# Performance work log

Measured on AMD Instinct MI355X. Metric: run time of the kernel, lower is better.

## Reference

```python
import jax, jax.numpy as jnp
import numpy as np

N_HEADS = 8
EPS = 1e-8


def _build_gp_map():
    # Cl(4,1) geometric-product structure constants. Blade index = 5-bit mask,
    # e1..e5 = bits 0..4; metric (+,+,+,+,-): e5 (bit 4) squares to -1.
    def pc(n):
        return bin(n).count("1")
    g = np.zeros((32, 32, 32), np.float32)
    for a in range(32):
        for b in range(32):
            swaps = 0
            aa = a >> 1
            while aa:
                swaps += pc(aa & b)
                aa >>= 1
            sign = -1.0 if (swaps & 1) else 1.0
            if (a & b) & 0b10000:  # shared e5 factor contributes -1
                sign = -sign
            g[a, b, a ^ b] = sign
    return g

GP_MAP = jnp.asarray(_build_gp_map())          # (32,32,32)
BIVEC_IDX = jnp.array([3, 5, 6, 9, 10, 12, 17, 18, 20, 24])  # grade-2 blades
SCALAR_VECTOR_IDX = np.array([0, 1, 2, 4, 8, 16])            # grade-0 + grade-1


def normalize_cl41(x):
    return x / jnp.sqrt(jnp.sum(x * x, axis=-1, keepdims=True) + EPS)


def geometric_linear(w, x):
    # w: (O,I,32), x: (...,I,32) -> (...,O,32)
    wg = jnp.einsum('oij,jlk->oilk', w, GP_MAP)     # fold gp_map into weight
    out = jnp.einsum('oilk,...il->...ok', wg, x)
    return normalize_cl41(out)


def _init_weight(key, out_f, in_f):
    # Grade-aware Xavier: only scalar + vector lanes are nonzero.
    std = 1.0 / np.sqrt(in_f * 32)
    vals = jax.random.normal(key, (out_f, in_f, len(SCALAR_VECTOR_IDX)), jnp.float32) * std
    w = jnp.zeros((out_f, in_f, 32), jnp.float32)
    return w.at[:, :, SCALAR_VECTOR_IDX].set(vals)


def setup_inputs() -> dict:
    key = jax.random.key(0)
    kx, kq, kk, kv, ko = jax.random.split(key, 5)
    B, S, D = 2, 384, 128
    x = jax.random.normal(kx, (B, S, D, 32), jnp.float32)
    return {
        'x': x,
        'wq': _init_weight(kq, D, D),
        'wk': _init_weight(kk, D, D),
        'wv': _init_weight(kv, D, D),
        'wo': _init_weight(ko, D, D),
        'attn_lambda': jnp.float32(0.1),
    }


def reference(x, wq, wk, wv, wo, attn_lambda):
    B, S, D, _ = x.shape
    H = N_HEADS
    hd = D // H
    def split_heads(t):  # (B,S,D,32) -> (B,H,S,hd,32)
        return t.reshape(B, S, H, hd, 32).transpose(0, 2, 1, 3, 4)
    q = split_heads(geometric_linear(wq, x))
    k = split_heads(geometric_linear(wk, x))
    v = split_heads(geometric_linear(wv, x))

    # Geometric product Q*K contracted over head_dim, then over gp_map lanes.
    qg = jnp.einsum('bhsdi,ijk->bhsdjk', q, GP_MAP)      # (B,H,S,hd,32,32)
    raw_mv = jnp.einsum('bhsdjk,bhxdj->bhsxk', qg, k)    # (B,H,S,S,32)
    raw_mv = normalize_cl41(raw_mv)

    scalar_part = raw_mv[..., 0]
    biv = raw_mv[..., BIVEC_IDX]
    bivector_norm = jnp.sqrt(jnp.sum(biv * biv, axis=-1) + EPS)
    score = (scalar_part + attn_lambda * bivector_norm) / np.sqrt(hd).astype(np.float32)
    attn_probs = jax.nn.softmax(score, axis=-1)          # (B,H,S,S)

    out = jnp.einsum('bhsx,bhxdl->bhsdl', attn_probs, v)  # (B,H,S,hd,32)
    out = out.transpose(0, 2, 1, 3, 4).reshape(B, S, D, 32)
    return geometric_linear(wo, out)
```

## Files before the change

### kernel.cpp

```cpp
#include <hip/hip_runtime.h>
#include <math.h>

#define BB    2
#define SS    384
#define DD    128
#define NH    8
#define HDIM  16
#define NBH   16
#define BS    768

typedef unsigned int   u32;
typedef unsigned short u16;
typedef __attribute__((ext_vector_type(8))) short short8;
typedef __attribute__((ext_vector_type(4))) float f32x4;

struct SignTab { float v[32][32]; };
constexpr int popcnt32c(int x){ int c=0; for(int i=0;i<32;i++) c += (x>>i)&1; return c; }
constexpr int signgp_int(int a, int b){
  int swaps=0; int aa=a>>1;
  while(aa){ swaps += popcnt32c(aa & b); aa >>= 1; }
  int s = (swaps & 1) ? -1 : 1;
  if ((a & b) & 16) s = -s;
  return s;
}
constexpr SignTab make_signs(){
  SignTab t{};
  for(int a=0;a<32;a++) for(int b=0;b<32;b++)
    t.v[a][b] = (float)signgp_int(a,b);
  return t;
}
constexpr SignTab GPS = make_signs();

struct MaskTab { u32 v[4][8][4][4]; };
constexpr MaskTab mkmask(){
  MaskTab t{};
  for(int w=0;w<4;w++) for(int u=0;u<8;u++) for(int q=0;q<4;q++) for(int r=0;r<4;r++){
    u32 m = 0;
    for(int h=0;h<2;h++){
      int j = 2*r + h;
      int i = (q<<3) | j;
      int c = (w<<3) | u;
      if (signgp_int(i, i^c) < 0) m |= (h ? 0x80000000u : 0x8000u);
    }
    t.v[w][u][q][r] = m;
  }
  return t;
}
constexpr MaskTab MT = mkmask();

__device__ __forceinline__ u16 f2bf(float f){
  u32 x = __float_as_uint(f);
  return (u16)((x + 0x7FFFu + ((x>>16)&1u)) >> 16);
}
__device__ __forceinline__ float bf2f(u16 h){
  return __uint_as_float(((u32)h) << 16);
}

__global__ __launch_bounds__(256) void repack_wb(const float* __restrict__ wq,
                                                 const float* __restrict__ wk,
                                                 const float* __restrict__ wv,
                                                 const float* __restrict__ wo,
                                                 u16* __restrict__ wpk2){
  int idx = blockIdx.x*256 + threadIdx.x;
  int p = blockIdx.y;
  const float* w = (p==0)?wq:(p==1)?wk:(p==2)?wv:wo;
  int o   = idx / 768;
  int rem = idx - o*768;
  int jp  = rem >> 7;
  int i   = rem & 127;
  const int SV[6] = {0,1,2,4,8,16};
  wpk2[p*98304 + idx] = f2bf(w[(o*128 + i)*32 + SV[jp]]);
}

#define XLS 33
__global__ __launch_bounds__(256) void gather_k(const void* __restrict__ src,
                                                int src_bf16,
                                                u16* __restrict__ xg){
  __shared__ float xl[2*128*XLS];
  int t = threadIdx.x;
  int bs0 = blockIdx.x*2;
  int bsl = t >> 7, i = t & 127;

  float row[32];
  if (src_bf16){
    const uint4* s4 = (const uint4*)((const u16*)src + (((size_t)(bs0+bsl)*128 + i)*32));
    #pragma unroll
    for(int r=0;r<4;r++){
      uint4 v = s4[r];
      u32 ww[4] = {v.x,v.y,v.z,v.w};
      #pragma unroll
      for(int h=0;h<4;h++){
        row[r*8 + 2*h    ] = __uint_as_float(ww[h] << 16);
        row[r*8 + 2*h + 1] = __uint_as_float(ww[h] & 0xFFFF0000u);
      }
    }
  } else {
    const float4* s4 = (const float4*)((const float*)src + (((size_t)(bs0+bsl)*128 + i)*32));
    #pragma unroll
    for(int r=0;r<8;r++){
      float4 v = s4[r];
      row[r*4+0]=v.x; row[r*4+1]=v.y; row[r*4+2]=v.z; row[r*4+3]=v.w;
    }
  }
  float* xrow = xl + bsl*128*XLS + i*XLS;
  #pragma unroll
  for(int l=0;l<32;l++) xrow[l] = row[l];
  __syncthreads();

  const int SV[6] = {0,1,2,4,8,16};
  u32* xg32 = (u32*)xg;
  #pragma unroll 4
  for(int r=0;r<96;r++){
    int wr = t + r*256;
    int k   = wr / 768;
    int rem = wr - k*768;
    int bl  = rem / 384;
    int r2  = rem - bl*384;
    int jp  = r2 >> 6;
    int ip  = r2 & 63;
    int i2  = ip*2;
    int b   = SV[jp] ^ k;
    float sg = GPS.v[SV[jp]][b];
    const float* base = xl + bl*128*XLS;
    float f0 = base[ i2   *XLS + b] * sg;
    float f1 = base[(i2+1)*XLS + b] * sg;
    u32 pk = (u32)f2bf(f0) | ((u32)f2bf(f1) << 16);
    xg32[((size_t)k*768 + bs0 + bl)*384 + jp*64 + ip] = pk;
  }
}

#define LSTR 40
__global__ __launch_bounds__(256) void gemm_proj(const u16* __restrict__ xg,
                                                 const u16* __restrict__ wpkA,
                                                 u16* __restrict__ tmpA){
  __shared__ __align__(16) u16 As[128*LSTR];
  __shared__ __align__(16) u16 Bs[128*LSTR];
  int t = threadIdx.x;
  int Mt = blockIdx.x, k = blockIdx.y, p = blockIdx.z;
  const u16* wpk = wpkA + (size_t)p*98304;
  u16* tmp = tmpA + (size_t)p*32*768*128;

  int w = t >> 6, lane = t & 63;
  int q = lane >> 4, n16 = lane & 15;
  int wm = w >> 1, wn = w & 1;

  f32x4 acc[4][4];
  #pragma unroll
  for(int a=0;a<4;a++)
    #pragma unroll
    for(int b=0;b<4;b++) acc[a][b] = (f32x4){0.f,0.f,0.f,0.f};

  int r0 = t>>2, c0 = (t&3)*8;
  int r1 = (t+256)>>2, c1 = ((t+256)&3)*8;
  const u16* Aab = xg + ((size_t)k*768 + Mt*128)*768;

  uint4 pa0, pa1, pb0, pb1;
  {
    pa0 = *(const uint4*)(Aab + (size_t)r0*768 + c0);
    pa1 = *(const uint4*)(Aab + (size_t)r1*768 + c1);
    pb0 = *(const uint4*)(wpk + (size_t)r0*768 + c0);
    pb1 = *(const uint4*)(wpk + (size_t)r1*768 + c1);
  }

  for(int kt=0; kt<24; kt++){
    __syncthreads();
    *(uint4*)(As + r0*LSTR + c0) = pa0;
    *(uint4*)(As + r1*LSTR + c1) = pa1;
    *(uint4*)(Bs + r0*LSTR + c0) = pb0;
    *(uint4*)(Bs + r1*LSTR + c1) = pb1;
    __syncthreads();
    if (kt < 23){
      int kn = (kt+1)*32;
      pa0 = *(const uint4*)(Aab + (size_t)r0*768 + kn + c0);
      pa1 = *(const uint4*)(Aab + (size_t)r1*768 + kn + c1);
      pb0 = *(const uint4*)(wpk + (size_t)r0*768 + kn + c0);
      pb1 = *(const uint4*)(wpk + (size_t)r1*768 + kn + c1);
    }
    short8 a[4], b[4];
    #pragma unroll
    for(int mi=0;mi<4;mi++)
      a[mi] = *(const short8*)(As + (wm*64 + mi*16 + n16)*LSTR + q*8);
    #pragma unroll
    for(int ni=0;ni<4;ni++)
      b[ni] = *(const short8*)(Bs + (wn*64 + ni*16 + n16)*LSTR + q*8);
    #pragma unroll
    for(int mi=0;mi<4;mi++)
      #pragma unroll
      for(int ni=0;ni<4;ni++)
        acc[mi][ni] = __builtin_amdgcn_mfma_f32_16x16x32_bf16(a[mi], b[ni], acc[mi][ni], 0,0,0);
  }

  #pragma unroll
  for(int mi=0;mi<4;mi++){
    #pragma unroll
    for(int r=0;r<4;r++){
      int m = Mt*128 + wm*64 + mi*16 + q*4 + r;
      #pragma unroll
      for(int ni=0;ni<4;ni++){
        int n = wn*64 + ni*16 + n16;
        tmp[((size_t)k*768 + m)*128 + n] = f2bf(acc[mi][ni][r]);
      }
    }
  }
}

__global__ __launch_bounds__(256) void norm3(const u16* __restrict__ tmpA,
                                             u16* __restrict__ qhb,
                                             u16* __restrict__ khb,
                                             u16* __restrict__ vbb){
  int z = blockIdx.y;
  const u16* tmp = tmpA + (size_t)z*32*768*128;
  u16* dst = (z==0)?qhb:(z==1)?khb:vbb;
  int t = threadIdx.x;
  int bsl = t >> 7, o = t & 127;
  int bs = blockIdx.x*2 + bsl;

  float a[32];
  float ssum = 1e-8f;
  #pragma unroll
  for(int k=0;k<32;k++){
    a[k] = bf2f(tmp[((size_t)k*768 + bs)*128 + o]);
    ssum = fmaf(a[k], a[k], ssum);
  }
  float inv = 1.0f / sqrtf(ssum);

  int b = bs / SS, s = bs - b*SS;
  int h = o >> 4, d = o & 15;
  uint4* og4 = (uint4*)(dst + (((size_t)(b*NH + h)*SS + s)*512 + d*32));
  #pragma unroll
  for(int l=0;l<4;l++){
    uint4 v;
    v.x = (u32)f2bf(a[8*l+0]*inv) | ((u32)f2bf(a[8*l+1]*inv)<<16);
    v.y = (u32)f2bf(a[8*l+2]*inv) | ((u32)f2bf(a[8*l+3]*inv)<<16);
    v.z = (u32)f2bf(a[8*l+4]*inv) | ((u32)f2bf(a[8*l+5]*inv)<<16);
    v.w = (u32)f2bf(a[8*l+6]*inv) | ((u32)f2bf(a[8*l+7]*inv)<<16);
    og4[l] = v;
  }
}

__global__ __launch_bounds__(256) void norm_out(const u16* __restrict__ tmp,
                                                float* __restrict__ dst){
  int t = threadIdx.x;
  int bsl = t >> 7, o = t & 127;
  int bs = blockIdx.x*2 + bsl;

  float a[32];
  float ssum = 1e-8f;
  #pragma unroll
  for(int k=0;k<32;k++){
    a[k] = bf2f(tmp[((size_t)k*768 + bs)*128 + o]);
    ssum = fmaf(a[k], a[k], ssum);
  }
  float inv = 1.0f / sqrtf(ssum);
  float4* og = (float4*)(dst + ((size_t)bs*128 + o)*32);
  #pragma unroll
  for(int l4=0;l4<8;l4++){
    float4 v;
    v.x = a[4*l4+0]*inv; v.y = a[4*l4+1]*inv;
    v.z = a[4*l4+2]*inv; v.w = a[4*l4+3]*inv;
    og[l4] = v;
  }
}

#define TVS 528
__global__ __launch_bounds__(256) void transpose_v(const u16* __restrict__ vb,
                                                   u16* __restrict__ vt){
  __shared__ __align__(16) u16 vl[32*TVS];
  int t = threadIdx.x;
  int xt = blockIdx.x, bh = blockIdx.y;
  const u16* src = vb + ((size_t)bh*SS + xt*32)*512;
  #pragma unroll
  for(int j=0;j<8;j++){
    int f = t + j*256; int row = f>>6, c = (f&63)*8;
    *(uint4*)(vl + row*TVS + c) = *(const uint4*)(src + (size_t)row*512 + c);
  }
  __syncthreads();
  u16* dst = vt + (size_t)bh*512*SS + xt*32;
  #pragma unroll
  for(int j=0;j<8;j++){
    int f = t + j*256; int dl = f>>2, c4 = (f&3)*8;
    u16 tmp[8];
    #pragma unroll
    for(int e=0;e<8;e++) tmp[e] = vl[(c4+e)*TVS + dl];
    *(uint4*)(dst + (size_t)dl*SS + c4) = *(uint4*)tmp;
  }
}

#define QSTR 264
__global__ __launch_bounds__(256,2) void scores_mfma(const u16* __restrict__ qh,
                                                     const u16* __restrict__ kh,
                                                     float* __restrict__ sc,
                                                     const float* __restrict__ lam){
  __shared__ __align__(16) u16 smem[(64+16)*QSTR];
  u16* qs = smem;
  u16* ks = smem + 64*QSTR;
  int t = threadIdx.x;
  int xt = blockIdx.x, st = blockIdx.y, bh = blockIdx.z;
  int w = t >> 6, lane = t & 63, q = lane >> 4, mn = lane & 15;
  float lm = lam[0];

  u32 FM[8][4];
  #pragma unroll
  for(int u=0;u<8;u++)
    #pragma unroll
    for(int r=0;r<4;r++) FM[u][r] = MT.v[w][u][q][r];

  f32x4 acc[4][8];
  #pragma unroll
  for(int mi=0;mi<4;mi++)
    #pragma unroll
    for(int u=0;u<8;u++) acc[mi][u] = (f32x4){0.f,0.f,0.f,0.f};

  for(int h=0; h<2; h++){
    __syncthreads();
    const u16* qbase = qh + ((size_t)bh*SS + st*64)*512 + h*256;
    const u16* kbase = kh + ((size_t)bh*SS + xt*16)*512 + h*256;
    #pragma unroll
    for(int j=0;j<8;j++){
      int f = t + j*256;
      int row = f>>5, c = (f&31)*8;
      *(uint4*)(qs + row*QSTR + c) = *(const uint4*)(qbase + (size_t)row*512 + c);
    }
    #pragma unroll
    for(int j=0;j<2;j++){
      int f = t + j*256;
      int row = f>>5, c = (f&31)*8;
      *(uint4*)(ks + row*QSTR + c) = *(const uint4*)(kbase + (size_t)row*512 + c);
    }
    __syncthreads();

    for(int ktl=0; ktl<8; ktl++){
      short8 a[4];
      #pragma unroll
      for(int mi=0;mi<4;mi++)
        a[mi] = *(const short8*)(qs + (mi*16+mn)*QSTR + ktl*32 + q*8);
      uint4 khd = *(const uint4*)(ks + mn*QSTR + ktl*32 + ((q^w)<<3));
      u32 kk[4]  = {khd.x, khd.y, khd.z, khd.w};
      u32 kks[4];
      #pragma unroll
      for(int r=0;r<4;r++) kks[r] = (kk[r]>>16)|(kk[r]<<16);
      #pragma unroll
      for(int u=0;u<8;u++){
        union { u32 w32[4]; short8 s; } bf;
        #pragma unroll
        for(int r=0;r<4;r++){
          u32 v = (u & 1) ? kks[r ^ (u>>1)] : kk[r ^ (u>>1)];
          bf.w32[r] = v ^ FM[u][r];
        }
        #pragma unroll
        for(int mi=0;mi<4;mi++)
          acc[mi][u] = __builtin_amdgcn_mfma_f32_16x16x32_bf16(a[mi], bf.s, acc[mi][u], 0, 0, 0);
      }
    }
  }
  __syncthreads();

  float* pss = (float*)smem;
  float* pbb = pss + 64*68;
  float* ps0 = pbb + 64*68;

  #pragma unroll
  for(int mi=0;mi<4;mi++){
    #pragma unroll
    for(int rr=0;rr<4;rr++){
      float ssv = 0.f, bbv = 0.f;
      #pragma unroll
      for(int u=0;u<8;u++){
        int c = w*8 + u;
        bool isb = (c==3)||(c==5)||(c==6)||(c==9)||(c==10)||(c==12)||
                   (c==17)||(c==18)||(c==20)||(c==24);
        float v = acc[mi][u][rr];
        ssv = fmaf(v, v, ssv);
        if (isb) bbv = fmaf(v, v, bbv);
      }
      int s = mi*16 + q*4 + rr;
      pss[s*68 + w*16 + mn] = ssv;
      pbb[s*68 + w*16 + mn] = bbv;
      if (w == 0) ps0[s*17 + mn] = acc[mi][0][rr];
    }
  }
  __syncthreads();

  int x = t & 15, s0 = t >> 4;
  #pragma unroll
  for(int ssi=0; ssi<4; ssi++){
    int s = s0 + ssi*16;
    float ss = 1e-8f, bb = 0.f;
    #pragma unroll
    for(int ww=0; ww<4; ww++){
      ss += pss[s*68 + ww*16 + x];
      bb += pbb[s*68 + ww*16 + x];
    }
    float inv = 1.0f / sqrtf(ss);
    float s0v = ps0[s*17+x];
    float score = (s0v*inv + lm*sqrtf(bb*inv*inv + 1e-8f)) * 0.25f;
    sc[((size_t)bh*SS + st*64 + s)*SS + xt*16 + x] = score;
  }
}

#define PBS 392
#define VSS 40
__global__ __launch_bounds__(256,2) void pv_mfma(const float* __restrict__ sc,
                                                 const u16* __restrict__ vt,
                                                 u16* __restrict__ om){
  __shared__ __align__(16) u16 pb[16*PBS];
  __shared__ __align__(16) u16 vsm[512*VSS];
  int t = threadIdx.x;
  int st = blockIdx.x, bh = blockIdx.y;
  int w = t >> 6, lane = t & 63, q = lane >> 4, mn = lane & 15;

  {
    int row = t >> 4, g = t & 15;
    const float* srow = sc + ((size_t)bh*SS + st*16 + row)*SS;
    float v[24];
    float mx = -1e30f;
    #pragma unroll
    for(int k2=0;k2<24;k2++){ v[k2] = srow[g + k2*16]; mx = fmaxf(mx, v[k2]); }
    #pragma unroll
    for(int off=8; off; off>>=1) mx = fmaxf(mx, __shfl_xor(mx, off));
    float sum = 0.f;
    #pragma unroll
    for(int k2=0;k2<24;k2++){ v[k2] = __expf(v[k2]-mx); sum += v[k2]; }
    #pragma unroll
    for(int off=8; off; off>>=1) sum += __shfl_xor(sum, off);
    float inv = 1.f/sum;
    #pragma unroll
    for(int k2=0;k2<24;k2++) pb[row*PBS + g + k2*16] = f2bf(v[k2]*inv);
  }

  f32x4 acc[8];
  #pragma unroll
  for(int mt=0;mt<8;mt++) acc[mt] = (f32x4){0.f,0.f,0.f,0.f};

  const u16* vtb = vt + (size_t)bh*512*SS;
  for(int kt=0; kt<12; kt++){
    __syncthreads();
    #pragma unroll
    for(int j=0;j<8;j++){
      int f = t + j*256;
      int dl = f>>2, c4 = (f&3)*8;
      *(uint4*)(vsm + dl*VSS + c4) = *(const uint4*)(vtb + (size_t)dl*SS + kt*32 + c4);
    }
    __syncthreads();
    short8 b = *(const short8*)(pb + mn*PBS + kt*32 + q*8);
    #pragma unroll
    for(int mt=0;mt<8;mt++){
      short8 a = *(const short8*)(vsm + ((w*8+mt)*16 + mn)*VSS + q*8);
      acc[mt] = __builtin_amdgcn_mfma_f32_16x16x32_bf16(a, b, acc[mt], 0, 0, 0);
    }
  }
  __syncthreads();

  float* ot = (float*)vsm;
  #pragma unroll
  for(int mt=0;mt<8;mt++)
    #pragma unroll
    for(int rr=0;rr<4;rr++)
      ot[((w*8+mt)*16 + q*4 + rr)*17 + mn] = acc[mt][rr];
  __syncthreads();

  int b = bh >> 3, h = bh & 7;
  u32* om32 = (u32*)om;
  #pragma unroll
  for(int j=0;j<16;j++){
    int f = t + j*256;
    int s = f >> 8, dlp = f & 255, dl = dlp*2;
    float f0 = ot[dl*17 + s], f1 = ot[(dl+1)*17 + s];
    u32 pk = (u32)f2bf(f0) | ((u32)f2bf(f1) << 16);
    int sg = st*16 + s;
    om32[(size_t)(b*SS + sg)*2048 + h*256 + dlp] = pk;
  }
}

extern "C" void kernel_launch(void* const* d_in, const int* in_sizes, int n_in,
                              void* d_out, int out_size, void* d_ws, size_t ws_size,
                              hipStream_t stream) {
  const float* x   = (const float*)d_in[0];
  const float* wq  = (const float*)d_in[1];
  const float* wk  = (const float*)d_in[2];
  const float* wv  = (const float*)d_in[3];
  const float* wo  = (const float*)d_in[4];
  const float* lam = (const float*)d_in[5];
  float* out = (float*)d_out;

  char* ws = (char*)d_ws;
  size_t off = 0;
  u16*   wpk2 = (u16*)(ws + off); off += (size_t)4*98304*2;
  u16*   xg   = (u16*)(ws + off); off += (size_t)32*768*768*2;
  float* sc   = (float*)xg;
  u16*   tmp3 = (u16*)(ws + off); off += (size_t)3*32*768*128*2;
  u16*   vt   = tmp3;
  u16*   qhb  = (u16*)(ws + off); off += (size_t)NBH*SS*512*2;
  u16*   khb  = (u16*)(ws + off); off += (size_t)NBH*SS*512*2;
  u16*   vb   = (u16*)(ws + off); off += (size_t)NBH*SS*512*2;
  u16*   om   = (u16*)(ws + off); off += (size_t)BS*128*32*2;

  repack_wb<<<dim3(384,4),256,0,stream>>>(wq, wk, wv, wo, wpk2);
  gather_k<<<384,256,0,stream>>>(x, 0, xg);
  gemm_proj<<<dim3(6,32,3),256,0,stream>>>(xg, wpk2, tmp3);
  norm3<<<dim3(384,3),256,0,stream>>>(tmp3, qhb, khb, vb);
  transpose_v<<<dim3(12,16),256,0,stream>>>(vb, vt);

  scores_mfma<<<dim3(24,6,16),256,0,stream>>>(qhb, khb, sc, lam);
  pv_mfma<<<dim3(24,16),256,0,stream>>>(sc, vt, om);

  gather_k<<<384,256,0,stream>>>(om, 1, xg);
  gemm_proj<<<dim3(6,32,1),256,0,stream>>>(xg, wpk2 + (size_t)3*98304, tmp3);
  norm_out<<<384,256,0,stream>>>(tmp3, out);
}
```

Measured before the change: 265.5 us.

## Fuse weight repack into gather, fold output gather into PV, remap blocks per XCD

Merges the weight repack into the first gather launch, removing one kernel launch. The PV kernel now writes its output straight into the sign-applied gathered layout that the output projection GEMM expects, which removes the second gather kernel and the intermediate om buffer. The scores and PV grids are flattened and remapped so that blocks sharing a batch-head land on the same XCD, for better L2 locality. This adds scattered stores from PV and moves the scores buffer into the tmp3 region, so the aliasing must stay safe.

Result: faster. 254.5 us (-4.1%).

```diff
diff --git a/kernel.cpp b/kernel.cpp
--- a/kernel.cpp
+++ b/kernel.cpp
@@ -56,51 +56,39 @@
   return __uint_as_float(((u32)h) << 16);
 }
 
-__global__ __launch_bounds__(256) void repack_wb(const float* __restrict__ wq,
-                                                 const float* __restrict__ wk,
-                                                 const float* __restrict__ wv,
-                                                 const float* __restrict__ wo,
-                                                 u16* __restrict__ wpk2){
-  int idx = blockIdx.x*256 + threadIdx.x;
-  int p = blockIdx.y;
-  const float* w = (p==0)?wq:(p==1)?wk:(p==2)?wv:wo;
-  int o   = idx / 768;
-  int rem = idx - o*768;
-  int jp  = rem >> 7;
-  int i   = rem & 127;
-  const int SV[6] = {0,1,2,4,8,16};
-  wpk2[p*98304 + idx] = f2bf(w[(o*128 + i)*32 + SV[jp]]);
-}
-
 #define XLS 33
-__global__ __launch_bounds__(256) void gather_k(const void* __restrict__ src,
-                                                int src_bf16,
-                                                u16* __restrict__ xg){
+__global__ __launch_bounds__(256) void gather_k(const float* __restrict__ src,
+                                                u16* __restrict__ xg,
+                                                const float* __restrict__ wq,
+                                                const float* __restrict__ wk,
+                                                const float* __restrict__ wv,
+                                                const float* __restrict__ wo,
+                                                u16* __restrict__ wpk2){
+  if (blockIdx.y == 1){
+    int idx = blockIdx.x*256 + threadIdx.x;
+    int o   = idx / 768;
+    int rem = idx - o*768;
+    int jp  = rem >> 7;
+    int i   = rem & 127;
+    const int SV[6] = {0,1,2,4,8,16};
+    const float* ww[4] = {wq, wk, wv, wo};
+    #pragma unroll
+    for(int p=0;p<4;p++)
+      wpk2[p*98304 + idx] = f2bf(ww[p][(o*128 + i)*32 + SV[jp]]);
+    return;
+  }
+
   __shared__ float xl[2*128*XLS];
   int t = threadIdx.x;
   int bs0 = blockIdx.x*2;
   int bsl = t >> 7, i = t & 127;
 
   float row[32];
-  if (src_bf16){
-    const uint4* s4 = (const uint4*)((const u16*)src + (((size_t)(bs0+bsl)*128 + i)*32));
-    #pragma unroll
-    for(int r=0;r<4;r++){
-      uint4 v = s4[r];
-      u32 ww[4] = {v.x,v.y,v.z,v.w};
-      #pragma unroll
-      for(int h=0;h<4;h++){
-        row[r*8 + 2*h    ] = __uint_as_float(ww[h] << 16);
-        row[r*8 + 2*h + 1] = __uint_as_float(ww[h] & 0xFFFF0000u);
-      }
-    }
-  } else {
-    const float4* s4 = (const float4*)((const float*)src + (((size_t)(bs0+bsl)*128 + i)*32));
-    #pragma unroll
-    for(int r=0;r<8;r++){
-      float4 v = s4[r];
-      row[r*4+0]=v.x; row[r*4+1]=v.y; row[r*4+2]=v.z; row[r*4+3]=v.w;
-    }
+  const float4* s4 = (const float4*)(src + (((size_t)(bs0+bsl)*128 + i)*32));
+  #pragma unroll
+  for(int r=0;r<8;r++){
+    float4 v = s4[r];
+    row[r*4+0]=v.x; row[r*4+1]=v.y; row[r*4+2]=v.z; row[r*4+3]=v.w;
   }
   float* xrow = xl + bsl*128*XLS + i*XLS;
   #pragma unroll
@@ -295,7 +283,15 @@
   u16* qs = smem;
   u16* ks = smem + 64*QSTR;
   int t = threadIdx.x;
-  int xt = blockIdx.x, st = blockIdx.y, bh = blockIdx.z;
+  int id  = blockIdx.x;
+  int xcd = id & 7;
+  int g   = id >> 3;
+  int half= g / 144;
+  int r9  = g - half*144;
+  int bh  = xcd + 8*half;
+  int st  = r9 / 24;
+  int xt  = r9 - st*24;
+
   int w = t >> 6, lane = t & 63, q = lane >> 4, mn = lane & 15;
   float lm = lam[0];
 
@@ -402,20 +398,25 @@
 #define VSS 40
 __global__ __launch_bounds__(256,2) void pv_mfma(const float* __restrict__ sc,
                                                  const u16* __restrict__ vt,
-                                                 u16* __restrict__ om){
+                                                 u32* __restrict__ xgo){
   __shared__ __align__(16) u16 pb[16*PBS];
   __shared__ __align__(16) u16 vsm[512*VSS];
   int t = threadIdx.x;
-  int st = blockIdx.x, bh = blockIdx.y;
+  int id  = blockIdx.x;
+  int xcd = id & 7;
+  int g   = id >> 3;
+  int half= g / 24;
+  int st  = g - half*24;
+  int bh  = xcd + 8*half;
   int w = t >> 6, lane = t & 63, q = lane >> 4, mn = lane & 15;
 
   {
-    int row = t >> 4, g = t & 15;
+    int row = t >> 4, gg = t & 15;
     const float* srow = sc + ((size_t)bh*SS + st*16 + row)*SS;
     float v[24];
     float mx = -1e30f;
     #pragma unroll
-    for(int k2=0;k2<24;k2++){ v[k2] = srow[g + k2*16]; mx = fmaxf(mx, v[k2]); }
+    for(int k2=0;k2<24;k2++){ v[k2] = srow[gg + k2*16]; mx = fmaxf(mx, v[k2]); }
     #pragma unroll
     for(int off=8; off; off>>=1) mx = fmaxf(mx, __shfl_xor(mx, off));
     float sum = 0.f;
@@ -425,7 +426,7 @@
     for(int off=8; off; off>>=1) sum += __shfl_xor(sum, off);
     float inv = 1.f/sum;
     #pragma unroll
-    for(int k2=0;k2<24;k2++) pb[row*PBS + g + k2*16] = f2bf(v[k2]*inv);
+    for(int k2=0;k2<24;k2++) pb[row*PBS + gg + k2*16] = f2bf(v[k2]*inv);
   }
 
   f32x4 acc[8];
@@ -455,20 +456,30 @@
   #pragma unroll
   for(int mt=0;mt<8;mt++)
     #pragma unroll
-    for(int rr=0;rr<4;rr++)
-      ot[((w*8+mt)*16 + q*4 + rr)*17 + mn] = acc[mt][rr];
+    for(int rr=0;rr<4;rr++){
+      int dl = (w*8+mt)*16 + q*4 + rr;
+      int row = ((dl & 31) << 4) | (dl >> 5);
+      ot[row*17 + mn] = acc[mt][rr];
+    }
   __syncthreads();
 
   int b = bh >> 3, h = bh & 7;
-  u32* om32 = (u32*)om;
-  #pragma unroll
-  for(int j=0;j<16;j++){
-    int f = t + j*256;
-    int s = f >> 8, dlp = f & 255, dl = dlp*2;
-    float f0 = ot[dl*17 + s], f1 = ot[(dl+1)*17 + s];
-    u32 pk = (u32)f2bf(f0) | ((u32)f2bf(f1) << 16);
-    int sg = st*16 + s;
-    om32[(size_t)(b*SS + sg)*2048 + h*256 + dlp] = pk;
+  int bs_base = b*SS + st*16;
+  const int SVc[6] = {0,1,2,4,8,16};
+  #pragma unroll 4
+  for(int it=0; it<96; it++){
+    int idx = it*256 + t;
+    int dp = idx & 7;
+    int s  = (idx >> 3) & 15;
+    int jl = idx >> 7;
+    int jp = jl >> 5;
+    int l  = jl & 31;
+    int k  = SVc[jp] ^ l;
+    float sg = GPS.v[SVc[jp]][l];
+    float v0 = sg * ot[(l*16 + dp*2    )*17 + s];
+    float v1 = sg * ot[(l*16 + dp*2 + 1)*17 + s];
+    u32 pk = (u32)f2bf(v0) | ((u32)f2bf(v1) << 16);
+    xgo[((size_t)k*768 + bs_base + s)*384 + (size_t)(jp*64 + h*8 + dp)] = pk;
   }
 }
 
@@ -487,24 +498,21 @@
   size_t off = 0;
   u16*   wpk2 = (u16*)(ws + off); off += (size_t)4*98304*2;
   u16*   xg   = (u16*)(ws + off); off += (size_t)32*768*768*2;
-  float* sc   = (float*)xg;
   u16*   tmp3 = (u16*)(ws + off); off += (size_t)3*32*768*128*2;
   u16*   vt   = tmp3;
+  float* sc   = (float*)((char*)tmp3 + 6291456);
   u16*   qhb  = (u16*)(ws + off); off += (size_t)NBH*SS*512*2;
   u16*   khb  = (u16*)(ws + off); off += (size_t)NBH*SS*512*2;
   u16*   vb   = (u16*)(ws + off); off += (size_t)NBH*SS*512*2;
-  u16*   om   = (u16*)(ws + off); off += (size_t)BS*128*32*2;
-
-  repack_wb<<<dim3(384,4),256,0,stream>>>(wq, wk, wv, wo, wpk2);
-  gather_k<<<384,256,0,stream>>>(x, 0, xg);
+
+  gather_k<<<dim3(384,2),256,0,stream>>>(x, xg, wq, wk, wv, wo, wpk2);
   gemm_proj<<<dim3(6,32,3),256,0,stream>>>(xg, wpk2, tmp3);
   norm3<<<dim3(384,3),256,0,stream>>>(tmp3, qhb, khb, vb);
   transpose_v<<<dim3(12,16),256,0,stream>>>(vb, vt);
 
-  scores_mfma<<<dim3(24,6,16),256,0,stream>>>(qhb, khb, sc, lam);
-  pv_mfma<<<dim3(24,16),256,0,stream>>>(sc, vt, om);
-
-  gather_k<<<384,256,0,stream>>>(om, 1, xg);
+  scores_mfma<<<2304,256,0,stream>>>(qhb, khb, sc, lam);
+  pv_mfma<<<384,256,0,stream>>>(sc, vt, (u32*)xg);
+
   gemm_proj<<<dim3(6,32,1),256,0,stream>>>(xg, wpk2 + (size_t)3*98304, tmp3);
   norm_out<<<384,256,0,stream>>>(tmp3, out);
 }
```
